# Performance work log

Hardware: AMD Instinct MI355X
Metric: run time of the kernel (lower is better)

Reference implementation:

```python
import jax, jax.numpy as jnp
import numpy as np

B, H, N, D = 1, 12, 2048, 64
T = 8          # num_table
S = 256        # table_size
C = 8          # code_length = log2(S)
KQ = 4         # num_query_per_table (construct)
KV = 4         # num_query_per_table_val (query)


def setup_inputs() -> dict:
    key = jax.random.key(0)
    k1, k2, k3, k4 = jax.random.split(key, 4)
    return {
        "query_layer": jax.random.normal(k1, (B, H, N, D), jnp.float32),
        "key_layer": jax.random.normal(k2, (B, H, N, D), jnp.float32),
        "value_layer": jax.random.normal(k3, (B, H, N, D), jnp.float32),
        "attention_mask": jnp.ones((B, N), jnp.float32),
        "projections": jax.random.normal(k4, (H, T, C, D), jnp.float32) / np.sqrt(D).astype(np.float32),
    }


def _bucket_weights(scores):
    # scores: [BH, N, T, C] -> soft bucket weights [BH, N, T, S]
    p = jax.nn.sigmoid(scores)
    w = jnp.ones(scores.shape[:-1] + (1,), scores.dtype)
    for c in range(scores.shape[-1]):  # small fixed loop over code bits
        pc = p[..., c:c + 1]
        w = jnp.concatenate([w * (1.0 - pc), w * pc], axis=-1)
    return w  # bucket index bit order is internally consistent


def reference(query_layer, key_layer, value_layer, attention_mask, projections):
    BH = B * H
    # dense hash projections
    q_hash = jnp.einsum("bhnd,htcd->bhntc", query_layer, projections).reshape(BH, N, T, C)
    k_hash = jnp.einsum("bhnd,htcd->bhntc", key_layer, projections).reshape(BH, N, T, C)
    v = (value_layer * attention_mask[:, None, :, None]).reshape(BH, N, D)

    t_idx_q = jnp.broadcast_to(jnp.arange(T)[None, :, None], (N, T, KQ))
    t_idx_k = jnp.broadcast_to(jnp.arange(T)[None, :, None], (N, T, KV))

    # --- construct_tables: scatter weighted values into per-table buckets ---
    wq = _bucket_weights(q_hash)                 # [BH, N, T, S]
    tw, ti = jax.lax.top_k(wq, KQ)               # [BH, N, T, KQ]
    contrib = tw[..., None] * v[:, :, None, None, :]  # [BH, N, T, KQ, D]

    def scatter_b(ti_b, c_b):
        return jnp.zeros((T, S, D), v.dtype).at[t_idx_q, ti_b].add(c_b)

    tables = jax.vmap(scatter_b)(ti, contrib)    # [BH, T, S, D]

    # --- query_tables: gather buckets and weight-combine, average over tables ---
    wk = _bucket_weights(k_hash)                 # [BH, N, T, S]
    qw, qi = jax.lax.top_k(wk, KV)               # [BH, N, T, KV]

    def gather_b(tbl_b, qi_b, qw_b):
        g = tbl_b[t_idx_k, qi_b]                 # [N, T, KV, D]
        return jnp.einsum("ntk,ntkd->nd", qw_b, g)

    out = jax.vmap(gather_b)(tables, qi, qw) / T  # [BH, N, D]
    return out.reshape(B, H, N, D)
```

## Files before the change

### kernel.cpp

```cpp
#include <hip/hip_runtime.h>

#define HH   12
#define NN   2048
#define DD   64
#define TT   8
#define SS   256
#define KK   4
#define NHT  (HH * TT)

__device__ __forceinline__ int xcd_swz6144(int bid) {
  return (bid & 7) * 768 + (bid >> 3);
}

__device__ __forceinline__ void select_store(
    const float* __restrict__ s, int side, int ht, int n,
    float* __restrict__ selw, unsigned* __restrict__ selidx) {
  float p[8], qn[8];
  float dv[8]; int dc[8];
  int jbase = 0;
#pragma unroll
  for (int c = 0; c < 8; ++c) {
    p[c]  = 1.0f / (1.0f + expf(-s[c]));
    qn[c] = 1.0f - p[c];
    dv[c] = fabsf(s[c]); dc[c] = c;
    jbase |= (s[c] > 0.0f) ? (1 << c) : 0;
  }

#define CASX(i,j) { bool sw_ = dv[i] > dv[j];                         \
    float tv_ = sw_ ? dv[j] : dv[i]; float uv_ = sw_ ? dv[i] : dv[j]; \
    int   ti_ = sw_ ? dc[j] : dc[i]; int   ui_ = sw_ ? dc[i] : dc[j]; \
    dv[i] = tv_; dv[j] = uv_; dc[i] = ti_; dc[j] = ui_; }
  CASX(0,1) CASX(2,3) CASX(4,5) CASX(6,7)
  CASX(0,2) CASX(1,3) CASX(4,6) CASX(5,7)
  CASX(1,2) CASX(5,6)
  CASX(0,4) CASX(1,5) CASX(2,6) CASX(3,7)
  CASX(2,4) CASX(3,5)
  CASX(1,2) CASX(3,4) CASX(5,6)
#undef CASX

  int M1 = 1 << dc[0], M2 = 1 << dc[1], M3 = 1 << dc[2], M4 = 1 << dc[3];
  int cj[11] = { jbase,
                 jbase ^ M1, jbase ^ M2, jbase ^ M3, jbase ^ M4,
                 jbase ^ (M1|M2), jbase ^ (M1|M3), jbase ^ (M1|M4),
                 jbase ^ (M2|M3), jbase ^ (M2|M4), jbase ^ (M3|M4) };

  unsigned long long K0 = 0, K1 = 0, K2 = 0, K3 = 0;
#pragma unroll
  for (int kc = 0; kc < 11; ++kc) {
    int j = cj[kc];
    float w = (j & 1) ? p[0] : qn[0];
#pragma unroll
    for (int c = 1; c < 8; ++c) w *= ((j >> c) & 1) ? p[c] : qn[c];
    unsigned long long key =
        ((unsigned long long)__float_as_uint(w) << 32) | (unsigned)(255 - j);
    bool c0 = key > K0, c1 = key > K1, c2 = key > K2, c3 = key > K3;
    K3 = c2 ? K2 : (c3 ? key : K3);
    K2 = c1 ? K1 : (c2 ? key : K2);
    K1 = c0 ? K0 : (c1 ? key : K1);
    K0 = c0 ? key : K0;
  }

  float m0 = __uint_as_float((unsigned)(K0 >> 32));
  float m1 = __uint_as_float((unsigned)(K1 >> 32));
  float m2 = __uint_as_float((unsigned)(K2 >> 32));
  float m3 = __uint_as_float((unsigned)(K3 >> 32));
  int i0 = 255 - (int)(K0 & 255u);
  int i1 = 255 - (int)(K1 & 255u);
  int i2 = 255 - (int)(K2 & 255u);
  int i3 = 255 - (int)(K3 & 255u);

  size_t o = ((size_t)side * NHT + ht) * NN + n;
  ((float4*)selw)[o] = make_float4(m0, m1, m2, m3);
  selidx[o] = (unsigned)i0 | ((unsigned)i1 << 8) | ((unsigned)i2 << 16) | ((unsigned)i3 << 24);
}

__global__ __launch_bounds__(256) void select_topk(
    const float* __restrict__ q, const float* __restrict__ kx,
    const float* __restrict__ proj,
    float* __restrict__ selw, unsigned* __restrict__ selidx) {
  __shared__ float pj[64 * 68];
  __shared__ float xr[64 * 72];

  int b = blockIdx.x;
  int side = b / 384;
  int rem  = b - side * 384;
  int h    = rem >> 5;
  int n0   = (rem & 31) * 64;
  const float* src = side ? kx : q;

  for (int e4 = threadIdx.x; e4 < 1024; e4 += 256) {
    int e = e4 * 4;
    int t = e >> 9, c = (e >> 6) & 7, d4 = (e >> 2) & 15;
    float4 pv = ((const float4*)(proj + h * 4096))[e4];
    *(float4*)(&pj[(c * 8 + t) * 68 + d4 * 4]) = pv;
  }
  for (int e4 = threadIdx.x; e4 < 1024; e4 += 256) {
    int r = e4 >> 4, d4 = e4 & 15;
    float4 xv = ((const float4*)(src + ((size_t)h * NN + n0 + r) * DD))[d4];
    *(float4*)(&xr[r * 72 + d4 * 4]) = xv;
  }
  __syncthreads();

  int wave = threadIdx.x >> 6, lane = threadIdx.x & 63;
  int t = lane >> 3, rg = lane & 7;
  int rowa = wave * 16 + rg;
  int rowb = rowa + 8;

  float sa[8] = {0.f,0.f,0.f,0.f,0.f,0.f,0.f,0.f};
  float sb[8] = {0.f,0.f,0.f,0.f,0.f,0.f,0.f,0.f};
  const float* xa = &xr[rowa * 72];
  const float* xb = &xr[rowb * 72];
  for (int d0 = 0; d0 < 64; d0 += 4) {
    float4 xva = *(const float4*)(xa + d0);
    float4 xvb = *(const float4*)(xb + d0);
#pragma unroll
    for (int c = 0; c < 8; ++c) {
      float4 pv = *(const float4*)(&pj[(c * 8 + t) * 68 + d0]);
      sa[c] += xva.x * pv.x; sa[c] += xva.y * pv.y;
      sa[c] += xva.z * pv.z; sa[c] += xva.w * pv.w;
      sb[c] += xvb.x * pv.x; sb[c] += xvb.y * pv.y;
      sb[c] += xvb.z * pv.z; sb[c] += xvb.w * pv.w;
    }
  }

  int ht = h * TT + t;
  select_store(sa, side, ht, n0 + rowa, selw, selidx);
  select_store(sb, side, ht, n0 + rowb, selw, selidx);
}

__global__ __launch_bounds__(1024) void scan_scatter(
    const float* __restrict__ selw, const unsigned* __restrict__ selidx,
    const float* __restrict__ mask,
    unsigned* __restrict__ offsets, unsigned long long* __restrict__ entries) {
  __shared__ unsigned long long ebuf[NN * KK];
  __shared__ unsigned cur[SS];
  int ht = blockIdx.x;
  int tid = threadIdx.x;

  if (tid < SS) cur[tid] = 0;
  __syncthreads();

  for (int n = tid; n < NN; n += 1024) {
    unsigned ip = selidx[(size_t)ht * NN + n];
    atomicAdd(&cur[ip & 255u], 1u);
    atomicAdd(&cur[(ip >> 8) & 255u], 1u);
    atomicAdd(&cur[(ip >> 16) & 255u], 1u);
    atomicAdd(&cur[ip >> 24], 1u);
  }
  __syncthreads();

  if (tid < 64) {
    int lane = tid;
    unsigned c0 = cur[lane*4], c1 = cur[lane*4+1], c2 = cur[lane*4+2], c3 = cur[lane*4+3];
    unsigned sum = c0 + c1 + c2 + c3;
    unsigned x = sum;
#pragma unroll
    for (int off = 1; off <= 32; off <<= 1) {
      unsigned y = __shfl_up(x, off);
      if (lane >= off) x += y;
    }
    unsigned excl = x - sum;
    unsigned o0 = excl, o1 = excl + c0, o2 = o1 + c1, o3 = o2 + c2;
    cur[lane*4] = o0; cur[lane*4+1] = o1; cur[lane*4+2] = o2; cur[lane*4+3] = o3;
    unsigned* ob = offsets + (size_t)ht * SS;
    ob[lane*4] = o0; ob[lane*4+1] = o1; ob[lane*4+2] = o2; ob[lane*4+3] = o3;
  }
  __syncthreads();

  for (int n = tid; n < NN; n += 1024) {
    size_t o = (size_t)ht * NN + n;
    float4 w4 = ((const float4*)selw)[o];
    unsigned ip = selidx[o];
    float m = mask[n];
    unsigned b0 = ip & 255u, b1 = (ip >> 8) & 255u, b2 = (ip >> 16) & 255u, b3 = ip >> 24;
    unsigned s0 = atomicAdd(&cur[b0], 1u);
    ebuf[s0] = ((unsigned long long)__float_as_uint(w4.x * m) << 32) | (unsigned)n;
    unsigned s1 = atomicAdd(&cur[b1], 1u);
    ebuf[s1] = ((unsigned long long)__float_as_uint(w4.y * m) << 32) | (unsigned)n;
    unsigned s2 = atomicAdd(&cur[b2], 1u);
    ebuf[s2] = ((unsigned long long)__float_as_uint(w4.z * m) << 32) | (unsigned)n;
    unsigned s3 = atomicAdd(&cur[b3], 1u);
    ebuf[s3] = ((unsigned long long)__float_as_uint(w4.w * m) << 32) | (unsigned)n;
  }
  __syncthreads();

  unsigned long long* eb = entries + (size_t)ht * (NN * KK);
  for (int i = tid; i < NN * KK; i += 1024) eb[i] = ebuf[i];
}

__global__ __launch_bounds__(256) void build_tables(
    const float* __restrict__ v,
    const unsigned* __restrict__ offsets,
    const unsigned long long* __restrict__ entries,
    float* __restrict__ tables) {
  int wid = xcd_swz6144(blockIdx.x) * 4 + (threadIdx.x >> 6);
  int lane = threadIdx.x & 63;
  int ht = wid >> 8;
  int s  = wid & 255;
  int h  = ht >> 3;

  unsigned beg = offsets[(size_t)ht * SS + s];
  unsigned end = (s == SS - 1) ? (NN * KK) : offsets[(size_t)ht * SS + s + 1];
  unsigned cnt = end - beg;
  const unsigned long long* e = entries + (size_t)ht * (NN * KK) + beg;
  const float* vh = v + (size_t)h * NN * DD;

  float acc = 0.0f;
  unsigned i = 0;
  for (; i + 8 <= cnt; i += 8) {
    unsigned long long E0 = e[i],   E1 = e[i+1], E2 = e[i+2], E3 = e[i+3];
    unsigned long long E4 = e[i+4], E5 = e[i+5], E6 = e[i+6], E7 = e[i+7];
    float f0 = vh[(size_t)(unsigned)E0 * DD + lane];
    float f1 = vh[(size_t)(unsigned)E1 * DD + lane];
    float f2 = vh[(size_t)(unsigned)E2 * DD + lane];
    float f3 = vh[(size_t)(unsigned)E3 * DD + lane];
    float f4 = vh[(size_t)(unsigned)E4 * DD + lane];
    float f5 = vh[(size_t)(unsigned)E5 * DD + lane];
    float f6 = vh[(size_t)(unsigned)E6 * DD + lane];
    float f7 = vh[(size_t)(unsigned)E7 * DD + lane];
    acc = fmaf(__uint_as_float((unsigned)(E0 >> 32)), f0, acc);
    acc = fmaf(__uint_as_float((unsigned)(E1 >> 32)), f1, acc);
    acc = fmaf(__uint_as_float((unsigned)(E2 >> 32)), f2, acc);
    acc = fmaf(__uint_as_float((unsigned)(E3 >> 32)), f3, acc);
    acc = fmaf(__uint_as_float((unsigned)(E4 >> 32)), f4, acc);
    acc = fmaf(__uint_as_float((unsigned)(E5 >> 32)), f5, acc);
    acc = fmaf(__uint_as_float((unsigned)(E6 >> 32)), f6, acc);
    acc = fmaf(__uint_as_float((unsigned)(E7 >> 32)), f7, acc);
  }
  for (; i < cnt; ++i) {
    unsigned long long e0 = e[i];
    acc += __uint_as_float((unsigned)(e0 >> 32)) * vh[(size_t)(unsigned)e0 * DD + lane];
  }
  tables[(size_t)wid * DD + lane] = acc;
}

__global__ __launch_bounds__(256) void gather_out(
    const float* __restrict__ selw, const unsigned* __restrict__ selidx,
    const float* __restrict__ tables, float* __restrict__ out) {
  int wid = xcd_swz6144(blockIdx.x) * 4 + (threadIdx.x >> 6);
  int lane = threadIdx.x & 63;
  int h = wid >> 11;
  int n = wid & 2047;

  float4 w4[8]; unsigned ip[8];
#pragma unroll
  for (int t = 0; t < TT; ++t) {
    size_t o = ((size_t)NHT + (size_t)h * TT + t) * NN + n;
    w4[t] = ((const float4*)selw)[o];
    ip[t] = selidx[o];
  }
  float f[32];
#pragma unroll
  for (int t = 0; t < TT; ++t) {
    const float* tb = tables + ((size_t)h * TT + t) * SS * DD;
    f[t*4+0] = tb[(ip[t] & 255u) * DD + lane];
    f[t*4+1] = tb[((ip[t] >> 8) & 255u) * DD + lane];
    f[t*4+2] = tb[((ip[t] >> 16) & 255u) * DD + lane];
    f[t*4+3] = tb[(ip[t] >> 24) * DD + lane];
  }
  float acc = 0.0f;
#pragma unroll
  for (int t = 0; t < TT; ++t) {
    acc += w4[t].x * f[t*4+0];
    acc += w4[t].y * f[t*4+1];
    acc += w4[t].z * f[t*4+2];
    acc += w4[t].w * f[t*4+3];
  }
  out[((size_t)h * NN + n) * DD + lane] = acc * 0.125f;
}

extern "C" void kernel_launch(void* const* d_in, const int* in_sizes, int n_in,
                              void* d_out, int out_size, void* d_ws, size_t ws_size,
                              hipStream_t stream) {
  const float* q    = (const float*)d_in[0];
  const float* k    = (const float*)d_in[1];
  const float* v    = (const float*)d_in[2];
  const float* mask = (const float*)d_in[3];
  const float* proj = (const float*)d_in[4];
  float* out = (float*)d_out;

  float*    tables = (float*)d_ws;
  float*    selw   = tables + (size_t)NHT * SS * DD;
  unsigned* selidx = (unsigned*)(selw + (size_t)2 * NHT * NN * KK);
  unsigned* offsets = selidx + (size_t)2 * NHT * NN;
  unsigned long long* entries = (unsigned long long*)(offsets + (size_t)NHT * SS);

  select_topk<<<dim3(768), dim3(256), 0, stream>>>(q, k, proj, selw, selidx);
  scan_scatter<<<dim3(NHT), dim3(1024), 0, stream>>>(selw, selidx, mask, offsets, entries);
  build_tables<<<dim3(6144), dim3(256), 0, stream>>>(v, offsets, entries, tables);
  gather_out<<<dim3(6144), dim3(256), 0, stream>>>(selw, selidx, tables, out);
}
```

Baseline: 71.68 us.

## Split bucket scan into two half-sequence blocks and enlarge select_topk row tiles

The counting-sort scatter kernel now runs two blocks per (head,table), each handling half of the sequence with its own offsets and entry segment. This doubles its grid from 96 blocks and halves LDS use per block, so more CUs can work on it. build_tables now walks both segments per bucket. Separately, select_topk processes 128 rows per block with four accumulator sets per thread, halving the block count and reloading projections less often, at the cost of more registers and fewer blocks.

```diff
diff --git a/kernel.cpp b/kernel.cpp
--- a/kernel.cpp
+++ b/kernel.cpp
@@ -7,6 +7,7 @@
 #define SS   256
 #define KK   4
 #define NHT  (HH * TT)
+#define HALF 4096
 
 __device__ __forceinline__ int xcd_swz6144(int bid) {
   return (bid & 7) * 768 + (bid >> 3);
@@ -25,7 +26,6 @@
     dv[c] = fabsf(s[c]); dc[c] = c;
     jbase |= (s[c] > 0.0f) ? (1 << c) : 0;
   }
-
 #define CASX(i,j) { bool sw_ = dv[i] > dv[j];                         \
     float tv_ = sw_ ? dv[j] : dv[i]; float uv_ = sw_ ? dv[i] : dv[j]; \
     int   ti_ = sw_ ? dc[j] : dc[i]; int   ui_ = sw_ ? dc[i] : dc[j]; \
@@ -37,13 +37,11 @@
   CASX(2,4) CASX(3,5)
   CASX(1,2) CASX(3,4) CASX(5,6)
 #undef CASX
-
   int M1 = 1 << dc[0], M2 = 1 << dc[1], M3 = 1 << dc[2], M4 = 1 << dc[3];
   int cj[11] = { jbase,
                  jbase ^ M1, jbase ^ M2, jbase ^ M3, jbase ^ M4,
                  jbase ^ (M1|M2), jbase ^ (M1|M3), jbase ^ (M1|M4),
                  jbase ^ (M2|M3), jbase ^ (M2|M4), jbase ^ (M3|M4) };
-
   unsigned long long K0 = 0, K1 = 0, K2 = 0, K3 = 0;
 #pragma unroll
   for (int kc = 0; kc < 11; ++kc) {
@@ -59,7 +57,6 @@
     K1 = c0 ? K0 : (c1 ? key : K1);
     K0 = c0 ? key : K0;
   }
-
   float m0 = __uint_as_float((unsigned)(K0 >> 32));
   float m1 = __uint_as_float((unsigned)(K1 >> 32));
   float m2 = __uint_as_float((unsigned)(K2 >> 32));
@@ -68,7 +65,6 @@
   int i1 = 255 - (int)(K1 & 255u);
   int i2 = 255 - (int)(K2 & 255u);
   int i3 = 255 - (int)(K3 & 255u);
-
   size_t o = ((size_t)side * NHT + ht) * NN + n;
   ((float4*)selw)[o] = make_float4(m0, m1, m2, m3);
   selidx[o] = (unsigned)i0 | ((unsigned)i1 << 8) | ((unsigned)i2 << 16) | ((unsigned)i3 << 24);
@@ -79,13 +75,13 @@
     const float* __restrict__ proj,
     float* __restrict__ selw, unsigned* __restrict__ selidx) {
   __shared__ float pj[64 * 68];
-  __shared__ float xr[64 * 72];
+  __shared__ float xr[128 * 72];
 
   int b = blockIdx.x;
-  int side = b / 384;
-  int rem  = b - side * 384;
-  int h    = rem >> 5;
-  int n0   = (rem & 31) * 64;
+  int side = b / 192;
+  int rem  = b - side * 192;
+  int h    = rem >> 4;
+  int n0   = (rem & 15) * 128;
   const float* src = side ? kx : q;
 
   for (int e4 = threadIdx.x; e4 < 1024; e4 += 256) {
@@ -94,7 +90,7 @@
     float4 pv = ((const float4*)(proj + h * 4096))[e4];
     *(float4*)(&pj[(c * 8 + t) * 68 + d4 * 4]) = pv;
   }
-  for (int e4 = threadIdx.x; e4 < 1024; e4 += 256) {
+  for (int e4 = threadIdx.x; e4 < 2048; e4 += 256) {
     int r = e4 >> 4, d4 = e4 & 15;
     float4 xv = ((const float4*)(src + ((size_t)h * NN + n0 + r) * DD))[d4];
     *(float4*)(&xr[r * 72 + d4 * 4]) = xv;
@@ -103,45 +99,52 @@
 
   int wave = threadIdx.x >> 6, lane = threadIdx.x & 63;
   int t = lane >> 3, rg = lane & 7;
-  int rowa = wave * 16 + rg;
-  int rowb = rowa + 8;
-
-  float sa[8] = {0.f,0.f,0.f,0.f,0.f,0.f,0.f,0.f};
-  float sb[8] = {0.f,0.f,0.f,0.f,0.f,0.f,0.f,0.f};
-  const float* xa = &xr[rowa * 72];
-  const float* xb = &xr[rowb * 72];
+  int r0 = wave * 32 + rg;
+
+  float s0[8] = {0,0,0,0,0,0,0,0}, s1[8] = {0,0,0,0,0,0,0,0};
+  float s2[8] = {0,0,0,0,0,0,0,0}, s3[8] = {0,0,0,0,0,0,0,0};
+  const float* xa = &xr[(r0     ) * 72];
+  const float* xb = &xr[(r0 +  8) * 72];
+  const float* xc = &xr[(r0 + 16) * 72];
+  const float* xd = &xr[(r0 + 24) * 72];
   for (int d0 = 0; d0 < 64; d0 += 4) {
-    float4 xva = *(const float4*)(xa + d0);
-    float4 xvb = *(const float4*)(xb + d0);
+    float4 va = *(const float4*)(xa + d0);
+    float4 vb = *(const float4*)(xb + d0);
+    float4 vc = *(const float4*)(xc + d0);
+    float4 vd = *(const float4*)(xd + d0);
 #pragma unroll
     for (int c = 0; c < 8; ++c) {
       float4 pv = *(const float4*)(&pj[(c * 8 + t) * 68 + d0]);
-      sa[c] += xva.x * pv.x; sa[c] += xva.y * pv.y;
-      sa[c] += xva.z * pv.z; sa[c] += xva.w * pv.w;
-      sb[c] += xvb.x * pv.x; sb[c] += xvb.y * pv.y;
-      sb[c] += xvb.z * pv.z; sb[c] += xvb.w * pv.w;
+      s0[c] += va.x*pv.x; s0[c] += va.y*pv.y; s0[c] += va.z*pv.z; s0[c] += va.w*pv.w;
+      s1[c] += vb.x*pv.x; s1[c] += vb.y*pv.y; s1[c] += vb.z*pv.z; s1[c] += vb.w*pv.w;
+      s2[c] += vc.x*pv.x; s2[c] += vc.y*pv.y; s2[c] += vc.z*pv.z; s2[c] += vc.w*pv.w;
+      s3[c] += vd.x*pv.x; s3[c] += vd.y*pv.y; s3[c] += vd.z*pv.z; s3[c] += vd.w*pv.w;
     }
   }
 
   int ht = h * TT + t;
-  select_store(sa, side, ht, n0 + rowa, selw, selidx);
-  select_store(sb, side, ht, n0 + rowb, selw, selidx);
+  select_store(s0, side, ht, n0 + r0,      selw, selidx);
+  select_store(s1, side, ht, n0 + r0 + 8,  selw, selidx);
+  select_store(s2, side, ht, n0 + r0 + 16, selw, selidx);
+  select_store(s3, side, ht, n0 + r0 + 24, selw, selidx);
 }
 
 __global__ __launch_bounds__(1024) void scan_scatter(
     const float* __restrict__ selw, const unsigned* __restrict__ selidx,
     const float* __restrict__ mask,
     unsigned* __restrict__ offsets, unsigned long long* __restrict__ entries) {
-  __shared__ unsigned long long ebuf[NN * KK];
+  __shared__ unsigned long long ebuf[HALF];
   __shared__ unsigned cur[SS];
-  int ht = blockIdx.x;
+  int ht = blockIdx.x >> 1;
+  int g  = blockIdx.x & 1;
   int tid = threadIdx.x;
+  int nbase = g * 1024;
 
   if (tid < SS) cur[tid] = 0;
   __syncthreads();
 
-  for (int n = tid; n < NN; n += 1024) {
-    unsigned ip = selidx[(size_t)ht * NN + n];
+  {
+    unsigned ip = selidx[(size_t)ht * NN + nbase + tid];
     atomicAdd(&cur[ip & 255u], 1u);
     atomicAdd(&cur[(ip >> 8) & 255u], 1u);
     atomicAdd(&cur[(ip >> 16) & 255u], 1u);
@@ -162,30 +165,31 @@
     unsigned excl = x - sum;
     unsigned o0 = excl, o1 = excl + c0, o2 = o1 + c1, o3 = o2 + c2;
     cur[lane*4] = o0; cur[lane*4+1] = o1; cur[lane*4+2] = o2; cur[lane*4+3] = o3;
-    unsigned* ob = offsets + (size_t)ht * SS;
+    unsigned* ob = offsets + ((size_t)ht * 2 + g) * SS;
     ob[lane*4] = o0; ob[lane*4+1] = o1; ob[lane*4+2] = o2; ob[lane*4+3] = o3;
   }
   __syncthreads();
 
-  for (int n = tid; n < NN; n += 1024) {
+  {
+    int n = nbase + tid;
     size_t o = (size_t)ht * NN + n;
     float4 w4 = ((const float4*)selw)[o];
     unsigned ip = selidx[o];
     float m = mask[n];
     unsigned b0 = ip & 255u, b1 = (ip >> 8) & 255u, b2 = (ip >> 16) & 255u, b3 = ip >> 24;
-    unsigned s0 = atomicAdd(&cur[b0], 1u);
-    ebuf[s0] = ((unsigned long long)__float_as_uint(w4.x * m) << 32) | (unsigned)n;
-    unsigned s1 = atomicAdd(&cur[b1], 1u);
-    ebuf[s1] = ((unsigned long long)__float_as_uint(w4.y * m) << 32) | (unsigned)n;
-    unsigned s2 = atomicAdd(&cur[b2], 1u);
-    ebuf[s2] = ((unsigned long long)__float_as_uint(w4.z * m) << 32) | (unsigned)n;
-    unsigned s3 = atomicAdd(&cur[b3], 1u);
-    ebuf[s3] = ((unsigned long long)__float_as_uint(w4.w * m) << 32) | (unsigned)n;
-  }
-  __syncthreads();
-
-  unsigned long long* eb = entries + (size_t)ht * (NN * KK);
-  for (int i = tid; i < NN * KK; i += 1024) eb[i] = ebuf[i];
+    unsigned t0 = atomicAdd(&cur[b0], 1u);
+    ebuf[t0] = ((unsigned long long)__float_as_uint(w4.x * m) << 32) | (unsigned)n;
+    unsigned t1 = atomicAdd(&cur[b1], 1u);
+    ebuf[t1] = ((unsigned long long)__float_as_uint(w4.y * m) << 32) | (unsigned)n;
+    unsigned t2 = atomicAdd(&cur[b2], 1u);
+    ebuf[t2] = ((unsigned long long)__float_as_uint(w4.z * m) << 32) | (unsigned)n;
+    unsigned t3 = atomicAdd(&cur[b3], 1u);
+    ebuf[t3] = ((unsigned long long)__float_as_uint(w4.w * m) << 32) | (unsigned)n;
+  }
+  __syncthreads();
+
+  unsigned long long* eb = entries + ((size_t)ht * 2 + g) * HALF;
+  for (int i = tid; i < HALF; i += 1024) eb[i] = ebuf[i];
 }
 
 __global__ __launch_bounds__(256) void build_tables(
@@ -198,38 +202,41 @@
   int ht = wid >> 8;
   int s  = wid & 255;
   int h  = ht >> 3;
-
-  unsigned beg = offsets[(size_t)ht * SS + s];
-  unsigned end = (s == SS - 1) ? (NN * KK) : offsets[(size_t)ht * SS + s + 1];
-  unsigned cnt = end - beg;
-  const unsigned long long* e = entries + (size_t)ht * (NN * KK) + beg;
   const float* vh = v + (size_t)h * NN * DD;
 
   float acc = 0.0f;
-  unsigned i = 0;
-  for (; i + 8 <= cnt; i += 8) {
-    unsigned long long E0 = e[i],   E1 = e[i+1], E2 = e[i+2], E3 = e[i+3];
-    unsigned long long E4 = e[i+4], E5 = e[i+5], E6 = e[i+6], E7 = e[i+7];
-    float f0 = vh[(size_t)(unsigned)E0 * DD + lane];
-    float f1 = vh[(size_t)(unsigned)E1 * DD + lane];
-    float f2 = vh[(size_t)(unsigned)E2 * DD + lane];
-    float f3 = vh[(size_t)(unsigned)E3 * DD + lane];
-    float f4 = vh[(size_t)(unsigned)E4 * DD + lane];
-    float f5 = vh[(size_t)(unsigned)E5 * DD + lane];
-    float f6 = vh[(size_t)(unsigned)E6 * DD + lane];
-    float f7 = vh[(size_t)(unsigned)E7 * DD + lane];
-    acc = fmaf(__uint_as_float((unsigned)(E0 >> 32)), f0, acc);
-    acc = fmaf(__uint_as_float((unsigned)(E1 >> 32)), f1, acc);
-    acc = fmaf(__uint_as_float((unsigned)(E2 >> 32)), f2, acc);
-    acc = fmaf(__uint_as_float((unsigned)(E3 >> 32)), f3, acc);
-    acc = fmaf(__uint_as_float((unsigned)(E4 >> 32)), f4, acc);
-    acc = fmaf(__uint_as_float((unsigned)(E5 >> 32)), f5, acc);
-    acc = fmaf(__uint_as_float((unsigned)(E6 >> 32)), f6, acc);
-    acc = fmaf(__uint_as_float((unsigned)(E7 >> 32)), f7, acc);
-  }
-  for (; i < cnt; ++i) {
-    unsigned long long e0 = e[i];
-    acc += __uint_as_float((unsigned)(e0 >> 32)) * vh[(size_t)(unsigned)e0 * DD + lane];
+#pragma unroll
+  for (int g = 0; g < 2; ++g) {
+    const unsigned* ob = offsets + ((size_t)ht * 2 + g) * SS;
+    unsigned beg = ob[s];
+    unsigned end = (s == SS - 1) ? HALF : ob[s + 1];
+    unsigned cnt = end - beg;
+    const unsigned long long* e = entries + ((size_t)ht * 2 + g) * HALF + beg;
+    unsigned i = 0;
+    for (; i + 8 <= cnt; i += 8) {
+      unsigned long long E0 = e[i],   E1 = e[i+1], E2 = e[i+2], E3 = e[i+3];
+      unsigned long long E4 = e[i+4], E5 = e[i+5], E6 = e[i+6], E7 = e[i+7];
+      float f0 = vh[(size_t)(unsigned)E0 * DD + lane];
+      float f1 = vh[(size_t)(unsigned)E1 * DD + lane];
+      float f2 = vh[(size_t)(unsigned)E2 * DD + lane];
+      float f3 = vh[(size_t)(unsigned)E3 * DD + lane];
+      float f4 = vh[(size_t)(unsigned)E4 * DD + lane];
+      float f5 = vh[(size_t)(unsigned)E5 * DD + lane];
+      float f6 = vh[(size_t)(unsigned)E6 * DD + lane];
+      float f7 = vh[(size_t)(unsigned)E7 * DD + lane];
+      acc = fmaf(__uint_as_float((unsigned)(E0 >> 32)), f0, acc);
+      acc = fmaf(__uint_as_float((unsigned)(E1 >> 32)), f1, acc);
+      acc = fmaf(__uint_as_float((unsigned)(E2 >> 32)), f2, acc);
+      acc = fmaf(__uint_as_float((unsigned)(E3 >> 32)), f3, acc);
+      acc = fmaf(__uint_as_float((unsigned)(E4 >> 32)), f4, acc);
+      acc = fmaf(__uint_as_float((unsigned)(E5 >> 32)), f5, acc);
+      acc = fmaf(__uint_as_float((unsigned)(E6 >> 32)), f6, acc);
+      acc = fmaf(__uint_as_float((unsigned)(E7 >> 32)), f7, acc);
+    }
+    for (; i < cnt; ++i) {
+      unsigned long long e0 = e[i];
+      acc += __uint_as_float((unsigned)(e0 >> 32)) * vh[(size_t)(unsigned)e0 * DD + lane];
+    }
   }
   tables[(size_t)wid * DD + lane] = acc;
 }
@@ -283,10 +290,10 @@
   float*    selw   = tables + (size_t)NHT * SS * DD;
   unsigned* selidx = (unsigned*)(selw + (size_t)2 * NHT * NN * KK);
   unsigned* offsets = selidx + (size_t)2 * NHT * NN;
-  unsigned long long* entries = (unsigned long long*)(offsets + (size_t)NHT * SS);
-
-  select_topk<<<dim3(768), dim3(256), 0, stream>>>(q, k, proj, selw, selidx);
-  scan_scatter<<<dim3(NHT), dim3(1024), 0, stream>>>(selw, selidx, mask, offsets, entries);
+  unsigned long long* entries = (unsigned long long*)(offsets + (size_t)NHT * 2 * SS);
+
+  select_topk<<<dim3(384), dim3(256), 0, stream>>>(q, k, proj, selw, selidx);
+  scan_scatter<<<dim3(192), dim3(1024), 0, stream>>>(selw, selidx, mask, offsets, entries);
   build_tables<<<dim3(6144), dim3(256), 0, stream>>>(v, offsets, entries, tables);
   gather_out<<<dim3(6144), dim3(256), 0, stream>>>(selw, selidx, tables, out);
 }
```

Result: slower. 79.13 us (+10.4%).
